# Kernel tuning notes

Hardware: AMD Instinct MI355X
Metric: run time of the kernel (lower is better)

The kernel has to match this reference:

```python
import jax, jax.numpy as jnp
import numpy as np
import math

SEGMENT_LENGTHS = [2048, 4096, 8192]
DILATION_RATES = [1, 2, 4]


def setup_inputs() -> dict:
    key = jax.random.key(0)
    kq, kk, kv = jax.random.split(key, 3)
    b, n, h, d = 2, 8192, 32, 128
    q = jax.random.normal(kq, (b, n, h, d), dtype=jnp.float32)
    k = jax.random.normal(kk, (b, n, h, d), dtype=jnp.float32)
    v = jax.random.normal(kv, (b, n, h, d), dtype=jnp.float32)
    return {"q": q, "k": k, "v": v}


def _dilated_attention(q, k, v):
    # Faithful translation of _compute_dilated_attention.
    # NOTE: torch.matmul on (b, S, h, d) with transpose(-2, -1) contracts over
    # head_dim d and yields (b, S, h, h) scores: heads attend to heads at a
    # single (possibly dilated) key position. We reproduce that exactly.
    b, n, h, d = q.shape
    scale = 1.0 / math.sqrt(d)
    out = jnp.zeros_like(q)
    for seg_len, dil in zip(SEGMENT_LENGTHS, DILATION_RATES):
        if seg_len > n:
            continue
        n_seg = n // seg_len
        cov = n_seg * seg_len
        # (b, n_seg, seg_len, h, d)
        qs = q[:, :cov].reshape(b, n_seg, seg_len, h, d)
        if dil == 1:
            ks = k[:, :cov].reshape(b, n_seg, seg_len, h, d)
            vs = v[:, :cov].reshape(b, n_seg, seg_len, h, d)
        else:
            # idx[g, i] = g*seg_len + i*dil, clamped to n-1 (matches the loop)
            idx = (jnp.arange(n_seg)[:, None] * seg_len
                   + jnp.arange(seg_len)[None, :] * dil)
            idx = jnp.minimum(idx, n - 1)  # (n_seg, seg_len)
            ks = k[:, idx]  # (b, n_seg, seg_len, h, d)
            vs = v[:, idx]
        scores = jnp.einsum('bgsid,bgsjd->bgsij', qs, ks) * scale  # (b,g,s,h,h)
        attn = jax.nn.softmax(scores, axis=-1)
        res = jnp.einsum('bgsij,bgsjd->bgsid', attn, vs)
        # later configs overwrite earlier ones, as in the torch loop
        out = out.at[:, :cov].set(res.reshape(b, cov, h, d))
    return out


def reference(q, k, v):
    # world_size == 1 -> hierarchy level 1 -> _local_forward with all heads
    # local, which is just _compute_dilated_attention.
    return _dilated_attention(q, k, v)
```

## Files before the change

### kernel.cpp

```cpp
#include <hip/hip_runtime.h>
#include <hip/hip_bf16.h>

typedef __attribute__((ext_vector_type(4))) float f32x4;
typedef __attribute__((ext_vector_type(8))) __bf16 bf16x8;

#define NCTX 8192
#define DH 128
#define ROWE 4096
#define SC2 0.12751705766482797f
#define KSTR 136
#define PSTR 40
#define OSTR 132
#define BUFS (32*KSTR)

__device__ __forceinline__ unsigned f2bf(float x) {
  union { float f; unsigned u; } un; un.f = x;
  return (un.u + 0x7FFFu + ((un.u >> 16) & 1u)) >> 16;
}
__device__ __forceinline__ unsigned pk2(float a, float b) {
  float2 t; t.x = a; t.y = b;
  union { __hip_bfloat162 h; unsigned u; } un;
  un.h = __float22bfloat162_rn(t);
  return un.u;
}

__device__ __forceinline__ void stage_row(const float* __restrict__ src,
                                          unsigned short* dst, int lane) {
  const int jb = lane >> 5, d = 4 * (lane & 31);
#pragma unroll
  for (int half = 0; half < 2; ++half) {
    f32x4 x[8];
#pragma unroll
    for (int ch = 0; ch < 8; ++ch)
      x[ch] = *reinterpret_cast<const f32x4*>(src + 4*lane + 256*(half*8 + ch));
#pragma unroll
    for (int ch = 0; ch < 8; ++ch) {
      const int j = jb + 2*(half*8 + ch);
      uint2 wv;
      wv.x = pk2(x[ch][0], x[ch][1]);
      wv.y = pk2(x[ch][2], x[ch][3]);
      *reinterpret_cast<uint2*>(&dst[j*KSTR + d]) = wv;
    }
  }
}

__global__ __launch_bounds__(256, 2) void hda(
    const float* __restrict__ q, const float* __restrict__ kg,
    const float* __restrict__ v, float* __restrict__ out)
{
  extern __shared__ __align__(16) unsigned short lds[];

  const int tid  = threadIdx.x;
  const int w    = tid >> 6;
  const int lane = tid & 63;
  const int c = lane & 15;
  const int g = lane >> 4;

  const int pos = blockIdx.x * 4 + w;
  const int b = pos >> 13;
  const int s = pos & (NCTX - 1);
  const int s0 = (blockIdx.x * 4) & (NCTX - 1);
  const bool shared_kv = (s0 >= 2048);

  const float* qb_ = q  + (size_t)b * NCTX * ROWE;
  const float* kb_ = kg + (size_t)b * NCTX * ROWE;
  const float* vb_ = v  + (size_t)b * NCTX * ROWE;
  float*       op  = out + ((size_t)b * NCTX + s) * ROWE;

  unsigned short* sb = lds + w * BUFS;
  unsigned short* vbuf = shared_kv ? (lds + 5*BUFS) : (lds + (4 + w)*BUFS);
  const unsigned short* kbuf = shared_kv ? (lds + 4*BUFS) : sb;

  if (shared_kv) {
    const float* kr8 = kb_ + (size_t)(NCTX - 1) * ROWE;
    const float* vr8 = vb_ + (size_t)(NCTX - 1) * ROWE;
    const int d = 4 * (tid & 31), jb = tid >> 5;
#pragma unroll
    for (int ch = 0; ch < 4; ++ch) {
      const int fo = 4*tid + 1024*ch;
      const int j  = jb + 8*ch;
      f32x4 xk = *reinterpret_cast<const f32x4*>(kr8 + fo);
      f32x4 xv = *reinterpret_cast<const f32x4*>(vr8 + fo);
      uint2 wk, wv2;
      wk.x  = pk2(xk[0], xk[1]); wk.y  = pk2(xk[2], xk[3]);
      wv2.x = pk2(xv[0], xv[1]); wv2.y = pk2(xv[2], xv[3]);
      *reinterpret_cast<uint2*>(&lds[4*BUFS + j*KSTR + d]) = wk;
      *reinterpret_cast<uint2*>(&lds[5*BUFS + j*KSTR + d]) = wv2;
    }
    __syncthreads();
  }

  stage_row(qb_ + (size_t)s * ROWE, sb, lane);
  bf16x8 qa[2][4];
#pragma unroll
  for (int t = 0; t < 2; ++t)
#pragma unroll
    for (int ks = 0; ks < 4; ++ks)
      qa[t][ks] = *reinterpret_cast<const bf16x8*>(&sb[(t*16 + c)*KSTR + ks*32 + g*8]);

  if (!shared_kv)
    stage_row(kb_ + (size_t)(4*s) * ROWE, sb, lane);
  bf16x8 kf[2][4];
#pragma unroll
  for (int t = 0; t < 2; ++t)
#pragma unroll
    for (int ks = 0; ks < 4; ++ks)
      kf[t][ks] = *reinterpret_cast<const bf16x8*>(&kbuf[(t*16 + c)*KSTR + ks*32 + g*8]);

  if (!shared_kv)
    stage_row(vb_ + (size_t)(4*s) * ROWE, vbuf, lane);

  f32x4 S[2][2];
#pragma unroll
  for (int it = 0; it < 2; ++it)
#pragma unroll
    for (int jt = 0; jt < 2; ++jt) {
      f32x4 acc = (f32x4)0.0f;
#pragma unroll
      for (int ks = 0; ks < 4; ++ks)
        acc = __builtin_amdgcn_mfma_f32_16x16x32_bf16(qa[it][ks], kf[jt][ks], acc, 0, 0, 0);
      S[it][jt] = acc;
    }

  float p[2][2][4], inv[2][4];
#pragma unroll
  for (int it = 0; it < 2; ++it) {
    float ls[4] = {0.f, 0.f, 0.f, 0.f};
#pragma unroll
    for (int jt = 0; jt < 2; ++jt)
#pragma unroll
      for (int rr = 0; rr < 4; ++rr) {
        float e = exp2f(S[it][jt][rr] * SC2);
        p[it][jt][rr] = e;
        ls[rr] += e;
      }
#pragma unroll
    for (int m = 1; m <= 8; m <<= 1)
#pragma unroll
      for (int rr = 0; rr < 4; ++rr)
        ls[rr] += __shfl_xor(ls[rr], m);
#pragma unroll
    for (int rr = 0; rr < 4; ++rr) inv[it][rr] = 1.0f / ls[rr];
  }

#pragma unroll
  for (int it = 0; it < 2; ++it)
#pragma unroll
    for (int jt = 0; jt < 2; ++jt)
#pragma unroll
      for (int rr = 0; rr < 4; ++rr)
        sb[(it*16 + g*4 + rr)*PSTR + jt*16 + c] =
            (unsigned short)f2bf(p[it][jt][rr] * inv[it][rr]);

  bf16x8 pa[2];
  pa[0] = *reinterpret_cast<const bf16x8*>(&sb[c*PSTR + g*8]);
  pa[1] = *reinterpret_cast<const bf16x8*>(&sb[(16 + c)*PSTR + g*8]);

  bf16x8 va[8];
#pragma unroll
  for (int dt = 0; dt < 8; ++dt) {
    unsigned t0 = vbuf[(g*8 + 0)*KSTR + dt*16 + c];
    unsigned t1 = vbuf[(g*8 + 1)*KSTR + dt*16 + c];
    unsigned t2 = vbuf[(g*8 + 2)*KSTR + dt*16 + c];
    unsigned t3 = vbuf[(g*8 + 3)*KSTR + dt*16 + c];
    unsigned t4 = vbuf[(g*8 + 4)*KSTR + dt*16 + c];
    unsigned t5 = vbuf[(g*8 + 5)*KSTR + dt*16 + c];
    unsigned t6 = vbuf[(g*8 + 6)*KSTR + dt*16 + c];
    unsigned t7 = vbuf[(g*8 + 7)*KSTR + dt*16 + c];
    union { unsigned u[4]; bf16x8 f; } un;
    un.u[0] = t0 | (t1 << 16); un.u[1] = t2 | (t3 << 16);
    un.u[2] = t4 | (t5 << 16); un.u[3] = t6 | (t7 << 16);
    va[dt] = un.f;
  }

  float* ob = reinterpret_cast<float*>(sb);
#pragma unroll
  for (int it = 0; it < 2; ++it) {
    f32x4 o[8];
#pragma unroll
    for (int dt = 0; dt < 8; ++dt)
      o[dt] = __builtin_amdgcn_mfma_f32_16x16x32_bf16(va[dt], pa[it], (f32x4)0.0f, 0, 0, 0);
#pragma unroll
    for (int dt = 0; dt < 8; ++dt)
      *reinterpret_cast<f32x4*>(&ob[c*OSTR + dt*16 + g*4]) = o[dt];
#pragma unroll
    for (int ch = 0; ch < 8; ++ch) {
      const int flat = 4*lane + 256*ch;
      const int row = flat >> 7, col = flat & 127;
      f32x4 y = *reinterpret_cast<const f32x4*>(&ob[row*OSTR + col]);
      *reinterpret_cast<f32x4*>(op + it*2048 + flat) = y;
    }
  }
}

extern "C" void kernel_launch(void* const* d_in, const int* in_sizes, int n_in,
                              void* d_out, int out_size, void* d_ws, size_t ws_size,
                              hipStream_t stream) {
  const float* q = (const float*)d_in[0];
  const float* k = (const float*)d_in[1];
  const float* v = (const float*)d_in[2];
  float* o = (float*)d_out;
  hda<<<dim3(4096, 1, 1), dim3(256, 1, 1), 8 * BUFS * 2, stream>>>(q, k, v, o);
}
```

Measured before the change: 130.8 us.

## Process two positions per wave with Q prefetch and shared LDS buffer

Each wave now handles two consecutive sequence positions, and the grid is halved to match. The next position's Q row is loaded into registers while the current one is processed. K and V staging now reuse the wave's own LDS buffer instead of a separate per-wave V buffer. That cuts LDS per block from 8 to 6 buffers, and launch bounds are raised to allow 3 blocks per CU. The aim is to hide global load latency and raise occupancy, at the cost of more register pressure from the 16-register Q prefetch.

```diff
diff --git a/kernel.cpp b/kernel.cpp
--- a/kernel.cpp
+++ b/kernel.cpp
@@ -12,6 +12,7 @@
 #define PSTR 40
 #define OSTR 132
 #define BUFS (32*KSTR)
+#define PPW 2
 
 __device__ __forceinline__ unsigned f2bf(float x) {
   union { float f; unsigned u; } un; un.f = x;
@@ -44,7 +45,7 @@
   }
 }
 
-__global__ __launch_bounds__(256, 2) void hda(
+__global__ __launch_bounds__(256, 3) void hda(
     const float* __restrict__ q, const float* __restrict__ kg,
     const float* __restrict__ v, float* __restrict__ out)
 {
@@ -56,20 +57,20 @@
   const int c = lane & 15;
   const int g = lane >> 4;
 
-  const int pos = blockIdx.x * 4 + w;
-  const int b = pos >> 13;
-  const int s = pos & (NCTX - 1);
-  const int s0 = (blockIdx.x * 4) & (NCTX - 1);
-  const bool shared_kv = (s0 >= 2048);
+  const int p0 = (blockIdx.x * 4 + w) * PPW;
+  const int b  = p0 >> 13;
+  const int sbase = p0 & (NCTX - 1);
+  const int sblk  = (blockIdx.x * 4 * PPW) & (NCTX - 1);
+  const bool shared_kv = (sblk >= 2048);
 
   const float* qb_ = q  + (size_t)b * NCTX * ROWE;
   const float* kb_ = kg + (size_t)b * NCTX * ROWE;
   const float* vb_ = v  + (size_t)b * NCTX * ROWE;
-  float*       op  = out + ((size_t)b * NCTX + s) * ROWE;
+  float*       ob_ = out + (size_t)b * NCTX * ROWE;
 
   unsigned short* sb = lds + w * BUFS;
-  unsigned short* vbuf = shared_kv ? (lds + 5*BUFS) : (lds + (4 + w)*BUFS);
   const unsigned short* kbuf = shared_kv ? (lds + 4*BUFS) : sb;
+  const unsigned short* vbuf = shared_kv ? (lds + 5*BUFS) : sb;
 
   if (shared_kv) {
     const float* kr8 = kb_ + (size_t)(NCTX - 1) * ROWE;
@@ -90,105 +91,135 @@
     __syncthreads();
   }
 
-  stage_row(qb_ + (size_t)s * ROWE, sb, lane);
-  bf16x8 qa[2][4];
-#pragma unroll
-  for (int t = 0; t < 2; ++t)
-#pragma unroll
-    for (int ks = 0; ks < 4; ++ks)
-      qa[t][ks] = *reinterpret_cast<const bf16x8*>(&sb[(t*16 + c)*KSTR + ks*32 + g*8]);
-
-  if (!shared_kv)
-    stage_row(kb_ + (size_t)(4*s) * ROWE, sb, lane);
-  bf16x8 kf[2][4];
-#pragma unroll
-  for (int t = 0; t < 2; ++t)
-#pragma unroll
-    for (int ks = 0; ks < 4; ++ks)
-      kf[t][ks] = *reinterpret_cast<const bf16x8*>(&kbuf[(t*16 + c)*KSTR + ks*32 + g*8]);
-
-  if (!shared_kv)
-    stage_row(vb_ + (size_t)(4*s) * ROWE, vbuf, lane);
-
-  f32x4 S[2][2];
-#pragma unroll
-  for (int it = 0; it < 2; ++it)
-#pragma unroll
-    for (int jt = 0; jt < 2; ++jt) {
-      f32x4 acc = (f32x4)0.0f;
+  f32x4 qraw[16];
+#pragma unroll
+  for (int ch = 0; ch < 16; ++ch)
+    qraw[ch] = *reinterpret_cast<const f32x4*>(
+        qb_ + (size_t)sbase * ROWE + 4*lane + 256*ch);
+  __builtin_amdgcn_sched_barrier(0);
+
+#pragma unroll
+  for (int i = 0; i < PPW; ++i) {
+    const int s = sbase + i;
+
+    {
+      const int jb = lane >> 5, d = 4 * (lane & 31);
+#pragma unroll
+      for (int ch = 0; ch < 16; ++ch) {
+        uint2 wv;
+        wv.x = pk2(qraw[ch][0], qraw[ch][1]);
+        wv.y = pk2(qraw[ch][2], qraw[ch][3]);
+        *reinterpret_cast<uint2*>(&sb[(jb + 2*ch)*KSTR + d]) = wv;
+      }
+    }
+    bf16x8 qa[2][4];
+#pragma unroll
+    for (int t = 0; t < 2; ++t)
 #pragma unroll
       for (int ks = 0; ks < 4; ++ks)
-        acc = __builtin_amdgcn_mfma_f32_16x16x32_bf16(qa[it][ks], kf[jt][ks], acc, 0, 0, 0);
-      S[it][jt] = acc;
-    }
-
-  float p[2][2][4], inv[2][4];
-#pragma unroll
-  for (int it = 0; it < 2; ++it) {
-    float ls[4] = {0.f, 0.f, 0.f, 0.f};
-#pragma unroll
-    for (int jt = 0; jt < 2; ++jt)
-#pragma unroll
-      for (int rr = 0; rr < 4; ++rr) {
-        float e = exp2f(S[it][jt][rr] * SC2);
-        p[it][jt][rr] = e;
-        ls[rr] += e;
+        qa[t][ks] = *reinterpret_cast<const bf16x8*>(&sb[(t*16 + c)*KSTR + ks*32 + g*8]);
+
+    if (i + 1 < PPW) {
+#pragma unroll
+      for (int ch = 0; ch < 16; ++ch)
+        qraw[ch] = *reinterpret_cast<const f32x4*>(
+            qb_ + (size_t)(s + 1) * ROWE + 4*lane + 256*ch);
+      __builtin_amdgcn_sched_barrier(0);
+    }
+
+    if (!shared_kv)
+      stage_row(kb_ + (size_t)(4*s) * ROWE, sb, lane);
+    bf16x8 kf[2][4];
+#pragma unroll
+    for (int t = 0; t < 2; ++t)
+#pragma unroll
+      for (int ks = 0; ks < 4; ++ks)
+        kf[t][ks] = *reinterpret_cast<const bf16x8*>(&kbuf[(t*16 + c)*KSTR + ks*32 + g*8]);
+
+    if (!shared_kv)
+      stage_row(vb_ + (size_t)(4*s) * ROWE, sb, lane);
+
+    f32x4 S[2][2];
+#pragma unroll
+    for (int it = 0; it < 2; ++it)
+#pragma unroll
+      for (int jt = 0; jt < 2; ++jt) {
+        f32x4 acc = (f32x4)0.0f;
+#pragma unroll
+        for (int ks = 0; ks < 4; ++ks)
+          acc = __builtin_amdgcn_mfma_f32_16x16x32_bf16(qa[it][ks], kf[jt][ks], acc, 0, 0, 0);
+        S[it][jt] = acc;
       }
-#pragma unroll
-    for (int m = 1; m <= 8; m <<= 1)
-#pragma unroll
-      for (int rr = 0; rr < 4; ++rr)
-        ls[rr] += __shfl_xor(ls[rr], m);
-#pragma unroll
-    for (int rr = 0; rr < 4; ++rr) inv[it][rr] = 1.0f / ls[rr];
-  }
-
-#pragma unroll
-  for (int it = 0; it < 2; ++it)
-#pragma unroll
-    for (int jt = 0; jt < 2; ++jt)
-#pragma unroll
-      for (int rr = 0; rr < 4; ++rr)
-        sb[(it*16 + g*4 + rr)*PSTR + jt*16 + c] =
-            (unsigned short)f2bf(p[it][jt][rr] * inv[it][rr]);
-
-  bf16x8 pa[2];
-  pa[0] = *reinterpret_cast<const bf16x8*>(&sb[c*PSTR + g*8]);
-  pa[1] = *reinterpret_cast<const bf16x8*>(&sb[(16 + c)*PSTR + g*8]);
-
-  bf16x8 va[8];
-#pragma unroll
-  for (int dt = 0; dt < 8; ++dt) {
-    unsigned t0 = vbuf[(g*8 + 0)*KSTR + dt*16 + c];
-    unsigned t1 = vbuf[(g*8 + 1)*KSTR + dt*16 + c];
-    unsigned t2 = vbuf[(g*8 + 2)*KSTR + dt*16 + c];
-    unsigned t3 = vbuf[(g*8 + 3)*KSTR + dt*16 + c];
-    unsigned t4 = vbuf[(g*8 + 4)*KSTR + dt*16 + c];
-    unsigned t5 = vbuf[(g*8 + 5)*KSTR + dt*16 + c];
-    unsigned t6 = vbuf[(g*8 + 6)*KSTR + dt*16 + c];
-    unsigned t7 = vbuf[(g*8 + 7)*KSTR + dt*16 + c];
-    union { unsigned u[4]; bf16x8 f; } un;
-    un.u[0] = t0 | (t1 << 16); un.u[1] = t2 | (t3 << 16);
-    un.u[2] = t4 | (t5 << 16); un.u[3] = t6 | (t7 << 16);
-    va[dt] = un.f;
-  }
-
-  float* ob = reinterpret_cast<float*>(sb);
-#pragma unroll
-  for (int it = 0; it < 2; ++it) {
-    f32x4 o[8];
-#pragma unroll
-    for (int dt = 0; dt < 8; ++dt)
-      o[dt] = __builtin_amdgcn_mfma_f32_16x16x32_bf16(va[dt], pa[it], (f32x4)0.0f, 0, 0, 0);
-#pragma unroll
-    for (int dt = 0; dt < 8; ++dt)
-      *reinterpret_cast<f32x4*>(&ob[c*OSTR + dt*16 + g*4]) = o[dt];
-#pragma unroll
-    for (int ch = 0; ch < 8; ++ch) {
-      const int flat = 4*lane + 256*ch;
-      const int row = flat >> 7, col = flat & 127;
-      f32x4 y = *reinterpret_cast<const f32x4*>(&ob[row*OSTR + col]);
-      *reinterpret_cast<f32x4*>(op + it*2048 + flat) = y;
+
+    float p[2][2][4], inv[2][4];
+#pragma unroll
+    for (int it = 0; it < 2; ++it) {
+      float ls[4] = {0.f, 0.f, 0.f, 0.f};
+#pragma unroll
+      for (int jt = 0; jt < 2; ++jt)
+#pragma unroll
+        for (int rr = 0; rr < 4; ++rr) {
+          float e = exp2f(S[it][jt][rr] * SC2);
+          p[it][jt][rr] = e;
+          ls[rr] += e;
+        }
+#pragma unroll
+      for (int m = 1; m <= 8; m <<= 1)
+#pragma unroll
+        for (int rr = 0; rr < 4; ++rr)
+          ls[rr] += __shfl_xor(ls[rr], m);
+#pragma unroll
+      for (int rr = 0; rr < 4; ++rr) inv[it][rr] = 1.0f / ls[rr];
+    }
+
+    bf16x8 va[8];
+#pragma unroll
+    for (int dt = 0; dt < 8; ++dt) {
+      unsigned t0 = vbuf[(g*8 + 0)*KSTR + dt*16 + c];
+      unsigned t1 = vbuf[(g*8 + 1)*KSTR + dt*16 + c];
+      unsigned t2 = vbuf[(g*8 + 2)*KSTR + dt*16 + c];
+      unsigned t3 = vbuf[(g*8 + 3)*KSTR + dt*16 + c];
+      unsigned t4 = vbuf[(g*8 + 4)*KSTR + dt*16 + c];
+      unsigned t5 = vbuf[(g*8 + 5)*KSTR + dt*16 + c];
+      unsigned t6 = vbuf[(g*8 + 6)*KSTR + dt*16 + c];
+      unsigned t7 = vbuf[(g*8 + 7)*KSTR + dt*16 + c];
+      union { unsigned u[4]; bf16x8 f; } un;
+      un.u[0] = t0 | (t1 << 16); un.u[1] = t2 | (t3 << 16);
+      un.u[2] = t4 | (t5 << 16); un.u[3] = t6 | (t7 << 16);
+      va[dt] = un.f;
+    }
+
+#pragma unroll
+    for (int it = 0; it < 2; ++it)
+#pragma unroll
+      for (int jt = 0; jt < 2; ++jt)
+#pragma unroll
+        for (int rr = 0; rr < 4; ++rr)
+          sb[(it*16 + g*4 + rr)*PSTR + jt*16 + c] =
+              (unsigned short)f2bf(p[it][jt][rr] * inv[it][rr]);
+
+    bf16x8 pa[2];
+    pa[0] = *reinterpret_cast<const bf16x8*>(&sb[c*PSTR + g*8]);
+    pa[1] = *reinterpret_cast<const bf16x8*>(&sb[(16 + c)*PSTR + g*8]);
+
+    float* op = ob_ + (size_t)s * ROWE;
+    float* ob = reinterpret_cast<float*>(sb);
+#pragma unroll
+    for (int it = 0; it < 2; ++it) {
+      f32x4 o[8];
+#pragma unroll
+      for (int dt = 0; dt < 8; ++dt)
+        o[dt] = __builtin_amdgcn_mfma_f32_16x16x32_bf16(va[dt], pa[it], (f32x4)0.0f, 0, 0, 0);
+#pragma unroll
+      for (int dt = 0; dt < 8; ++dt)
+        *reinterpret_cast<f32x4*>(&ob[c*OSTR + dt*16 + g*4]) = o[dt];
+#pragma unroll
+      for (int ch = 0; ch < 8; ++ch) {
+        const int flat = 4*lane + 256*ch;
+        const int row = flat >> 7, col = flat & 127;
+        f32x4 y = *reinterpret_cast<const f32x4*>(&ob[row*OSTR + col]);
+        *reinterpret_cast<f32x4*>(op + it*2048 + flat) = y;
+      }
     }
   }
 }
@@ -200,5 +231,5 @@
   const float* k = (const float*)d_in[1];
   const float* v = (const float*)d_in[2];
   float* o = (float*)d_out;
-  hda<<<dim3(4096, 1, 1), dim3(256, 1, 1), 8 * BUFS * 2, stream>>>(q, k, v, o);
-}
+  hda<<<dim3(2048, 1, 1), dim3(256, 1, 1), 6 * BUFS * 2, stream>>>(q, k, v, o);
+}
```

Measured after the change: 145.3 us. 11.1% more time.
